# Performance work log

Measured on AMD Instinct MI355X. Metric: run time of the kernel, lower is better.

The kernel has to match this reference:

```python
import jax, jax.numpy as jnp
import numpy as np

N_NODES = 25000
N_HEDGES = 12500
NNZ = 400000
C_IN = 128
HID = 256
HEADS = 4
DH = HID // HEADS  # 64
NQ = 1             # number_queries
LN_EPS = 1e-5


def _layer_norm(x, g, b):
    m = jnp.mean(x, axis=-1, keepdims=True)
    v = jnp.mean((x - m) ** 2, axis=-1, keepdims=True)
    return (x - m) * jax.lax.rsqrt(v + LN_EPS) * g + b


def _block(x_src, src, tgt, n_tgt, K, Qw, V, ln0_g, ln0_b, ln1_g, ln1_b, W1, W2):
    """AllSetTransformerBlock: segment-softmax multi-head attention + LN/MLP.

    x_src: [N_src, C]; K,V: [H, C, DH]; Qw: [H, NQ, DH]; src,tgt: [E] int.
    torch.sparse.softmax over dim=1 == softmax over each target's incident
    sources (unspecified entries are -inf), so a segment softmax is exact.
    """
    xK = jnp.einsum('nc,hcd->hnd', x_src, K)        # [H, N, DH]
    alpha = jnp.einsum('hqd,hnd->nhq', Qw, xK)      # [N, H, NQ]
    a = alpha[src]                                   # [E, H, NQ] gather per incidence
    m = jax.ops.segment_max(a, tgt, num_segments=n_tgt)
    e = jnp.exp(a - m[tgt])
    den = jax.ops.segment_sum(e, tgt, num_segments=n_tgt)
    attn = e / den[tgt]                              # [E, H, NQ]
    v = jnp.einsum('nc,hcd->nhd', x_src, V)[src]     # [E, H, DH]
    w = attn[:, :, :, None] * v[:, :, None, :]       # [E, H, NQ, DH]
    out = jax.ops.segment_sum(w, tgt, num_segments=n_tgt)  # [T, H, NQ, DH]
    out = out + Qw[None]                             # residual with queries
    out = out.transpose(0, 2, 1, 3).reshape(n_tgt, NQ, HID)
    x = _layer_norm(out, ln0_g, ln0_b)
    h = jnp.maximum(x @ W1, 0.0) @ W2                # MLP: Linear-ReLU-Linear, no bias
    x = _layer_norm(x + jnp.maximum(h, 0.0), ln1_g, ln1_b)
    return x.sum(axis=1)                             # [T, HID]


def setup_inputs() -> dict:
    key = jax.random.key(0)
    ks = jax.random.split(key, 12)
    # injective linear-congruential index generation -> unique (node, hedge) pairs,
    # matching a coalesced sparse incidence matrix
    P = 15485863
    lin = (np.arange(NNZ, dtype=np.int64) * P) % (N_NODES * N_HEDGES)
    node_idx = jnp.asarray(lin // N_HEDGES, dtype=jnp.int64)
    hedge_idx = jnp.asarray(lin % N_HEDGES, dtype=jnp.int64)
    s = 0.05
    w = lambda k, shape: jax.random.normal(k, shape, jnp.float32) * s
    d = {
        'x0': jax.random.normal(ks[0], (N_NODES, C_IN), jnp.float32),
        'node_idx': node_idx,
        'hedge_idx': hedge_idx,
        'n_hedges': N_HEDGES,
        'v2e_K': w(ks[1], (HEADS, C_IN, DH)),
        'v2e_Q': w(ks[2], (HEADS, NQ, DH)),
        'v2e_V': w(ks[3], (HEADS, C_IN, DH)),
        'v2e_W1': w(ks[4], (HID, HID)),
        'v2e_W2': w(ks[5], (HID, HID)),
        'v2e_ln0_g': jnp.ones(HID, jnp.float32), 'v2e_ln0_b': jnp.zeros(HID, jnp.float32),
        'v2e_ln1_g': jnp.ones(HID, jnp.float32), 'v2e_ln1_b': jnp.zeros(HID, jnp.float32),
        'e2v_K': w(ks[6], (HEADS, HID, DH)),
        'e2v_Q': w(ks[7], (HEADS, NQ, DH)),
        'e2v_V': w(ks[8], (HEADS, HID, DH)),
        'e2v_W1': w(ks[9], (HID, HID)),
        'e2v_W2': w(ks[10], (HID, HID)),
        'e2v_ln0_g': jnp.ones(HID, jnp.float32), 'e2v_ln0_b': jnp.zeros(HID, jnp.float32),
        'e2v_ln1_g': jnp.ones(HID, jnp.float32), 'e2v_ln1_b': jnp.zeros(HID, jnp.float32),
    }
    return d


def reference(x0, node_idx, hedge_idx, n_hedges,
              v2e_K, v2e_Q, v2e_V, v2e_W1, v2e_W2,
              v2e_ln0_g, v2e_ln0_b, v2e_ln1_g, v2e_ln1_b,
              e2v_K, e2v_Q, e2v_V, e2v_W1, e2v_W2,
              e2v_ln0_g, e2v_ln0_b, e2v_ln1_g, e2v_ln1_b):
    n_nodes = x0.shape[0]
    # vertex -> hyperedge (neighborhood = B^T: targets are hyperedges)
    x1 = jax.nn.relu(_block(x0, node_idx, hedge_idx, n_hedges,
                            v2e_K, v2e_Q, v2e_V,
                            v2e_ln0_g, v2e_ln0_b, v2e_ln1_g, v2e_ln1_b,
                            v2e_W1, v2e_W2))
    # hyperedge -> vertex (neighborhood = B: targets are nodes)
    x0_out = jax.nn.relu(_block(x1, hedge_idx, node_idx, n_nodes,
                                e2v_K, e2v_Q, e2v_V,
                                e2v_ln0_g, e2v_ln0_b, e2v_ln1_g, e2v_ln1_b,
                                e2v_W1, e2v_W2))
    return x0_out, x1
```

## Files before the change

### kernel.cpp

```cpp
#include <hip/hip_runtime.h>
#include <hip/hip_bf16.h>

#define N_NODES_C 25000
#define N_HEDGES_C 12500
#define NNZ_C 400000
#define C_IN_C 128
#define HID_C 256
#define LN_EPS_C 1e-5f
#define CSR_STRIDE 64

typedef unsigned short ushort_t;
typedef __attribute__((ext_vector_type(8))) short short8;
typedef __attribute__((ext_vector_type(4))) float f32x4;

union U4S8 { uint4 u; short8 s; };

__device__ __forceinline__ float ldsel(const void* p, size_t i, bool f32) {
    return f32 ? ((const float*)p)[i] : __bfloat162float(((const __hip_bfloat16*)p)[i]);
}
__device__ __forceinline__ int ldidx(const void* p, size_t i, bool i64) {
    return i64 ? (int)((const long long*)p)[i] : ((const int*)p)[i];
}
__device__ __forceinline__ ushort_t bfbits(float f) {
    union { float f; unsigned u; } v; v.f = f;
    unsigned r = v.u + 0x7FFF + ((v.u >> 16) & 1);
    return (ushort_t)(r >> 16);
}
__device__ __forceinline__ float blo(unsigned u) {
    union { unsigned u; float f; } v; v.u = u << 16; return v.f;
}
__device__ __forceinline__ float bhi(unsigned u) {
    union { unsigned u; float f; } v; v.u = u & 0xFFFF0000u; return v.f;
}

#define INIT_GRID 148
__global__ void __launch_bounds__(256)
init_kernel(const unsigned* __restrict__ x0w, const unsigned* __restrict__ idxw,
            int* __restrict__ flags, unsigned* __restrict__ cnts,
            unsigned* __restrict__ vb32, unsigned* __restrict__ ea32) {
    int bid = blockIdx.x;
    if (bid == 0) {
        __shared__ int cnt[2];
        int t = threadIdx.x;
        if (t < 2) cnt[t] = 0;
        __syncthreads();
        int c0 = 0, c1 = 0;
        for (int k = 0; k < 4; k++) {
            unsigned w = x0w[t * 4 + k];
            unsigned elo = (w >> 7) & 0xFF;
            if (elo >= 100 && elo <= 134) c0++;
            if (idxw[2 * (t * 4 + k) + 1] == 0) c1++;
        }
        atomicAdd(&cnt[0], c0);
        atomicAdd(&cnt[1], c1);
        __syncthreads();
        if (t == 0) {
            flags[0] = (cnt[0] < 512) ? 1 : 0;
            flags[1] = (cnt[1] >= 512) ? 1 : 0;
        }
        return;
    }
    int i = (bid - 1) * 256 + threadIdx.x;
    if (i < 37500) { cnts[i] = 0u; return; }
    i -= 37500;
    if (i < 128) { vb32[25000 * 128 + i] = 0u; return; }
    i -= 128;
    if (i < 4) ea32[100000 + i] = 0u;
}

#define FILL_CHUNK 1024
#define FILL_NCHUNK ((NNZ_C + FILL_CHUNK - 1) / FILL_CHUNK)
#define FILL_BLOCKS (8 * FILL_NCHUNK)
#define HSLICE_SZ 1563
#define NSLICE_SZ 3125
#define PREP_TOTAL 364544
#define PREP_BLOCKS ((PREP_TOTAL + 255) / 256)
#define PF_GRID (FILL_BLOCKS + PREP_BLOCKS)

__global__ void __launch_bounds__(256)
prep_fill_kernel(const void* __restrict__ node_idx, const void* __restrict__ hedge_idx,
                 int* __restrict__ fill_h, int* __restrict__ fill_n,
                 ushort_t* __restrict__ scsr_h, ushort_t* __restrict__ scsr_n,
                 const void* __restrict__ K1, const void* __restrict__ Q1,
                 const void* __restrict__ V1,
                 const void* __restrict__ K2, const void* __restrict__ Q2,
                 const void* __restrict__ V2,
                 const void* __restrict__ W1a, const void* __restrict__ W2a,
                 const void* __restrict__ W1b, const void* __restrict__ W2b,
                 const void* __restrict__ G0a, const void* __restrict__ B0a,
                 const void* __restrict__ G1a, const void* __restrict__ B1a,
                 const void* __restrict__ G0b, const void* __restrict__ B0b,
                 const void* __restrict__ G1b, const void* __restrict__ B1b,
                 const int* __restrict__ flags,
                 float* __restrict__ kq1, float* __restrict__ kq2,
                 ushort_t* __restrict__ Vt1b, ushort_t* __restrict__ Vt2b,
                 ushort_t* __restrict__ W1tA, ushort_t* __restrict__ W2tA,
                 ushort_t* __restrict__ W1tB, ushort_t* __restrict__ W2tB,
                 float* __restrict__ qgb1, float* __restrict__ ep1,
                 float* __restrict__ qgb2, float* __restrict__ ep2) {
    if (blockIdx.x < FILL_BLOCKS) {
        bool i64 = flags[1] != 0;
        int s = blockIdx.x & 7;
        int chunk = blockIdx.x >> 3;
        int e0 = chunk * FILL_CHUNK;
        int e1 = e0 + FILL_CHUNK; if (e1 > NNZ_C) e1 = NNZ_C;
        int hlo = s * HSLICE_SZ, hhi = hlo + HSLICE_SZ;
        int nlo = s * NSLICE_SZ, nhi = nlo + NSLICE_SZ;
        for (int e = e0 + threadIdx.x; e < e1; e += 256) {
            int nd = ldidx(node_idx, e, i64);
            int he = ldidx(hedge_idx, e, i64);
            if (he >= hlo && he < hhi) {
                int p = atomicAdd(&fill_h[he], 1);
                if (p < CSR_STRIDE) scsr_h[(he << 6) + p] = (ushort_t)nd;
            }
            if (nd >= nlo && nd < nhi) {
                int p = atomicAdd(&fill_n[nd], 1);
                if (p < CSR_STRIDE) scsr_n[(nd << 6) + p] = (ushort_t)he;
            }
        }
        return;
    }
    bool f32 = flags[0] != 0;
    size_t i = (size_t)(blockIdx.x - FILL_BLOCKS) * 256 + threadIdx.x;
    if (i >= PREP_TOTAL) return;
    if (i < 512) {
        int h = (int)(i >> 7), c = (int)(i & 127);
        float s = 0.f;
        for (int d = 0; d < 64; d++)
            s += ldsel(K1, (size_t)(h * 128 + c) * 64 + d, f32) * ldsel(Q1, h * 64 + d, f32);
        kq1[h * 128 + c] = s;
        return;
    }
    i -= 512;
    if (i < 1024) {
        int h = (int)(i >> 8), c = (int)(i & 255);
        float s = 0.f;
        for (int d = 0; d < 64; d++)
            s += ldsel(K2, (size_t)(h * 256 + c) * 64 + d, f32) * ldsel(Q2, h * 64 + d, f32);
        kq2[h * 256 + c] = s;
        return;
    }
    i -= 1024;
    if (i < 32768) {
        int j = (int)(i >> 7), c = (int)(i & 127);
        int h = j >> 6, d = j & 63;
        Vt1b[i] = bfbits(ldsel(V1, (size_t)(h * 128 + c) * 64 + d, f32));
        return;
    }
    i -= 32768;
    if (i < 65536) {
        int j = (int)(i >> 8), c = (int)(i & 255);
        int h = j >> 6, d = j & 63;
        Vt2b[i] = bfbits(ldsel(V2, (size_t)(h * 256 + c) * 64 + d, f32));
        return;
    }
    i -= 65536;
    if (i < 65536) { int n = (int)(i >> 8), k = (int)(i & 255);
        W1tA[i] = bfbits(ldsel(W1a, (size_t)k * 256 + n, f32)); return; }
    i -= 65536;
    if (i < 65536) { int n = (int)(i >> 8), k = (int)(i & 255);
        W2tA[i] = bfbits(ldsel(W2a, (size_t)k * 256 + n, f32)); return; }
    i -= 65536;
    if (i < 65536) { int n = (int)(i >> 8), k = (int)(i & 255);
        W1tB[i] = bfbits(ldsel(W1b, (size_t)k * 256 + n, f32)); return; }
    i -= 65536;
    if (i < 65536) { int n = (int)(i >> 8), k = (int)(i & 255);
        W2tB[i] = bfbits(ldsel(W2b, (size_t)k * 256 + n, f32)); return; }
    i -= 65536;
    {
        int which = (int)(i >> 8);
        int j = (int)(i & 255);
        const void* src; float* dst;
        switch (which) {
            case 0: src = Q1;  dst = qgb1;       break;
            case 1: src = G0a; dst = qgb1 + 256; break;
            case 2: src = B0a; dst = qgb1 + 512; break;
            case 3: src = G1a; dst = ep1;        break;
            case 4: src = B1a; dst = ep1 + 256;  break;
            case 5: src = Q2;  dst = qgb2;       break;
            case 6: src = G0b; dst = qgb2 + 256; break;
            case 7: src = B0b; dst = qgb2 + 512; break;
            case 8: src = G1b; dst = ep2;        break;
            default: src = B1b; dst = ep2 + 256;  break;
        }
        dst[j] = ldsel(src, j, f32);
    }
}

__global__ void __launch_bounds__(256)
gemm_x0_kernel(const void* __restrict__ x0, const int* __restrict__ flags,
               const ushort_t* __restrict__ Bt, ushort_t* __restrict__ C,
               int M, int K, const float* __restrict__ kq, float* __restrict__ ea) {
    __shared__ ushort_t As[64 * 72];
    __shared__ ushort_t Bs[128 * 72];
    __shared__ float kqs[512];
    bool f32 = flags[0] != 0;
    int tid = threadIdx.x;
    int w = tid >> 6, lane = tid & 63;
    int l15 = lane & 15, kg = lane >> 4;
    int wr = w >> 1, wc = w & 1;
    int row0 = blockIdx.x * 64, col0 = blockIdx.y * 128;
    bool doEa = (blockIdx.y == 0);
    kqs[tid] = kq[tid];
    kqs[256 + tid] = kq[256 + tid];
    __syncthreads();
    f32x4 acc[2][4] = {{{0.f,0.f,0.f,0.f},{0.f,0.f,0.f,0.f},{0.f,0.f,0.f,0.f},{0.f,0.f,0.f,0.f}},
                       {{0.f,0.f,0.f,0.f},{0.f,0.f,0.f,0.f},{0.f,0.f,0.f,0.f},{0.f,0.f,0.f,0.f}}};
    float hd[2][4] = {{0.f,0.f,0.f,0.f},{0.f,0.f,0.f,0.f}};
    int r_ = tid >> 3, ch = tid & 7;
    for (int k0 = 0; k0 < K; k0 += 64) {
#pragma unroll
        for (int p = 0; p < 2; p++) {
            int r = p * 32 + r_;
            uint4 av = {0u,0u,0u,0u};
            int gr = row0 + r;
            if (gr < M) {
                float fv[8];
                if (!f32) {
                    av = *(const uint4*)((const ushort_t*)x0 + (size_t)gr * K + k0 + ch * 8);
                    if (doEa) {
                        unsigned* uw = (unsigned*)&av;
#pragma unroll
                        for (int jj = 0; jj < 4; jj++) { fv[2 * jj] = blo(uw[jj]); fv[2 * jj + 1] = bhi(uw[jj]); }
                    }
                } else {
                    const float* ap = (const float*)x0 + (size_t)gr * K + k0 + ch * 8;
                    float4 f0 = *(const float4*)ap;
                    float4 f1 = *(const float4*)(ap + 4);
                    av.x = (unsigned)bfbits(f0.x) | ((unsigned)bfbits(f0.y) << 16);
                    av.y = (unsigned)bfbits(f0.z) | ((unsigned)bfbits(f0.w) << 16);
                    av.z = (unsigned)bfbits(f1.x) | ((unsigned)bfbits(f1.y) << 16);
                    av.w = (unsigned)bfbits(f1.z) | ((unsigned)bfbits(f1.w) << 16);
                    if (doEa) {
                        fv[0] = f0.x; fv[1] = f0.y; fv[2] = f0.z; fv[3] = f0.w;
                        fv[4] = f1.x; fv[5] = f1.y; fv[6] = f1.z; fv[7] = f1.w;
                    }
                }
                if (doEa) {
                    int c = k0 + ch * 8;
#pragma unroll
                    for (int h = 0; h < 4; h++) {
                        float s = 0.f;
#pragma unroll
                        for (int j = 0; j < 8; j++) s += fv[j] * kqs[h * 128 + c + j];
                        hd[p][h] += s;
                    }
                }
            }
            *(uint4*)&As[r * 72 + ch * 8] = av;
        }
#pragma unroll
        for (int p = 0; p < 4; p++) {
            int i = p * 256 + tid;
            int r2 = i >> 3, c2 = i & 7;
            uint4 bv = *(const uint4*)(Bt + (size_t)(col0 + r2) * K + k0 + c2 * 8);
            *(uint4*)&Bs[r2 * 72 + c2 * 8] = bv;
        }
        __syncthreads();
#pragma unroll
        for (int kk = 0; kk < 2; kk++) {
            U4S8 a0_, a1_;
            a0_.u = *(const uint4*)&As[(32 * wr + l15) * 72 + kk * 32 + kg * 8];
            a1_.u = *(const uint4*)&As[(32 * wr + 16 + l15) * 72 + kk * 32 + kg * 8];
#pragma unroll
            for (int n = 0; n < 4; n++) {
                U4S8 b; b.u = *(const uint4*)&Bs[(64 * wc + 16 * n + l15) * 72 + kk * 32 + kg * 8];
                acc[0][n] = __builtin_amdgcn_mfma_f32_16x16x32_bf16(a0_.s, b.s, acc[0][n], 0, 0, 0);
                acc[1][n] = __builtin_amdgcn_mfma_f32_16x16x32_bf16(a1_.s, b.s, acc[1][n], 0, 0, 0);
            }
        }
        __syncthreads();
    }
#pragma unroll
    for (int m = 0; m < 2; m++) {
#pragma unroll
        for (int n = 0; n < 4; n++) {
#pragma unroll
            for (int rr = 0; rr < 4; rr++) {
                int row = row0 + 32 * wr + 16 * m + kg * 4 + rr;
                if (row < M)
                    C[(size_t)row * 256 + col0 + 64 * wc + 16 * n + l15] = bfbits(acc[m][n][rr]);
            }
        }
    }
    if (doEa) {
#pragma unroll
        for (int p = 0; p < 2; p++) {
#pragma unroll
            for (int msk = 1; msk < 8; msk <<= 1) {
                hd[p][0] += __shfl_xor(hd[p][0], msk);
                hd[p][1] += __shfl_xor(hd[p][1], msk);
                hd[p][2] += __shfl_xor(hd[p][2], msk);
                hd[p][3] += __shfl_xor(hd[p][3], msk);
            }
            if (ch == 0) {
                int row = row0 + p * 32 + r_;
                if (row < M) {
                    float4 o;
                    o.x = __expf(hd[p][0]); o.y = __expf(hd[p][1]);
                    o.z = __expf(hd[p][2]); o.w = __expf(hd[p][3]);
                    *(float4*)(ea + (size_t)row * 4) = o;
                }
            }
        }
    }
}

#define LOADB4(SRC, KO) { \
    bv0 = *(const uint4*)((SRC) + (size_t)rb * 256 + (KO) + cb * 8); \
    bv1 = *(const uint4*)((SRC) + (size_t)(rb + 64) * 256 + (KO) + cb * 8); \
    bv2 = *(const uint4*)((SRC) + (size_t)(rb + 128) * 256 + (KO) + cb * 8); \
    bv3 = *(const uint4*)((SRC) + (size_t)(rb + 192) * 256 + (KO) + cb * 8); }
#define WRITEB4() { \
    *(uint4*)&Bs[rb * 72 + cb * 8] = bv0; \
    *(uint4*)&Bs[(rb + 64) * 72 + cb * 8] = bv1; \
    *(uint4*)&Bs[(rb + 128) * 72 + cb * 8] = bv2; \
    *(uint4*)&Bs[(rb + 192) * 72 + cb * 8] = bv3; }

__global__ void __launch_bounds__(512)
fused_mlp_ln_kernel(const ushort_t* __restrict__ A, const ushort_t* __restrict__ W1t,
                    const ushort_t* __restrict__ W2t, const float* __restrict__ ep,
                    float* __restrict__ outF, int M,
                    const ushort_t* __restrict__ Vt2b, const float* __restrict__ kq,
                    ushort_t* __restrict__ vbOut, float* __restrict__ eaOut,
                    unsigned* __restrict__ zrow, float* __restrict__ zea) {
    __shared__ ushort_t Bs[256 * 72];
    __shared__ ushort_t hs[32 * 264];
    __shared__ float s1s[32][4];
    __shared__ float s2s[32][4];
    __shared__ float kqs[1024];
    ushort_t* As = hs;
    int tid = threadIdx.x;
    int w = tid >> 6, lane = tid & 63;
    int l15 = lane & 15, kg = lane >> 4;
    int wr = w >> 2, wc = w & 3;
    int row0 = blockIdx.x * 32;
    bool dir1 = (Vt2b != nullptr);
    if (dir1) { kqs[tid] = kq[tid]; kqs[512 + tid] = kq[512 + tid]; }
    f32x4 acc[4] = {{0.f,0.f,0.f,0.f},{0.f,0.f,0.f,0.f},{0.f,0.f,0.f,0.f},{0.f,0.f,0.f,0.f}};
    int rb = tid >> 3, cb = tid & 7;
    bool doA = tid < 256;
    int gr = row0 + rb;
    uint4 av = {0u,0u,0u,0u};
    uint4 bv0, bv1, bv2, bv3;
    LOADB4(W1t, 0);
    if (doA && gr < M) av = *(const uint4*)(A + (size_t)gr * 256 + cb * 8);
    for (int k0 = 0; k0 < 256; k0 += 64) {
        WRITEB4();
        if (doA) *(uint4*)&As[rb * 72 + cb * 8] = av;
        __syncthreads();
        if (k0 < 192) {
            LOADB4(W1t, k0 + 64);
            if (doA && gr < M) av = *(const uint4*)(A + (size_t)gr * 256 + (k0 + 64) + cb * 8);
        }
#pragma unroll
        for (int kk = 0; kk < 2; kk++) {
            U4S8 a0_;
            a0_.u = *(const uint4*)&As[(16 * wr + l15) * 72 + kk * 32 + kg * 8];
#pragma unroll
            for (int n = 0; n < 4; n++) {
                U4S8 b; b.u = *(const uint4*)&Bs[(64 * wc + 16 * n + l15) * 72 + kk * 32 + kg * 8];
                acc[n] = __builtin_amdgcn_mfma_f32_16x16x32_bf16(a0_.s, b.s, acc[n], 0, 0, 0);
            }
        }
        __syncthreads();
    }
    LOADB4(W2t, 0);
#pragma unroll
    for (int n = 0; n < 4; n++) {
#pragma unroll
        for (int rr = 0; rr < 4; rr++) {
            int br = 16 * wr + kg * 4 + rr;
            hs[br * 264 + 64 * wc + 16 * n + l15] = bfbits(fmaxf(acc[n][rr], 0.f));
            acc[n][rr] = 0.f;
        }
    }
    __syncthreads();
    for (int k0 = 0; k0 < 256; k0 += 64) {
        WRITEB4();
        __syncthreads();
        if (k0 < 192) LOADB4(W2t, k0 + 64);
#pragma unroll
        for (int kk = 0; kk < 2; kk++) {
            U4S8 a0_;
            a0_.u = *(const uint4*)&hs[(16 * wr + l15) * 264 + k0 + kk * 32 + kg * 8];
#pragma unroll
            for (int n = 0; n < 4; n++) {
                U4S8 b; b.u = *(const uint4*)&Bs[(64 * wc + 16 * n + l15) * 72 + kk * 32 + kg * 8];
                acc[n] = __builtin_amdgcn_mfma_f32_16x16x32_bf16(a0_.s, b.s, acc[n], 0, 0, 0);
            }
        }
        __syncthreads();
    }
    float ym[4][4];
#pragma unroll
    for (int rr = 0; rr < 4; rr++) {
        int br = 16 * wr + kg * 4 + rr;
        int grow = row0 + br;
        float ls1 = 0.f;
#pragma unroll
        for (int n = 0; n < 4; n++) {
            int col = 64 * wc + 16 * n + l15;
            float xv = 0.f;
            if (grow < M) xv = blo((unsigned)A[(size_t)grow * 256 + col]);
            float yv = xv + fmaxf(acc[n][rr], 0.f);
            ym[n][rr] = yv;
            ls1 += yv;
        }
#pragma unroll
        for (int msk = 1; msk < 16; msk <<= 1) ls1 += __shfl_xor(ls1, msk);
        if (l15 == 0) s1s[br][wc] = ls1;
    }
    __syncthreads();
    float mean_[4];
#pragma unroll
    for (int rr = 0; rr < 4; rr++) {
        int br = 16 * wr + kg * 4 + rr;
        float mn = (s1s[br][0] + s1s[br][1] + s1s[br][2] + s1s[br][3]) * (1.f / 256.f);
        mean_[rr] = mn;
        float ls2 = 0.f;
#pragma unroll
        for (int n = 0; n < 4; n++) {
            float d = ym[n][rr] - mn;
            ls2 += d * d;
        }
#pragma unroll
        for (int msk = 1; msk < 16; msk <<= 1) ls2 += __shfl_xor(ls2, msk);
        if (l15 == 0) s2s[br][wc] = ls2;
    }
    __syncthreads();
#pragma unroll
    for (int rr = 0; rr < 4; rr++) {
        int br = 16 * wr + kg * 4 + rr;
        int grow = row0 + br;
        float var = (s2s[br][0] + s2s[br][1] + s2s[br][2] + s2s[br][3]) * (1.f / 256.f);
        float rs = rsqrtf(var + LN_EPS_C);
#pragma unroll
        for (int n = 0; n < 4; n++) {
            int col = 64 * wc + 16 * n + l15;
            float rv = (ym[n][rr] - mean_[rr]) * rs * ep[col] + ep[256 + col];
            rv = fmaxf(rv, 0.f);
            if (grow < M) outF[(size_t)grow * 256 + col] = rv;
            if (dir1) hs[br * 264 + col] = bfbits(rv);
        }
    }
    if (!dir1) return;
#pragma unroll
    for (int n = 0; n < 4; n++)
#pragma unroll
        for (int rr = 0; rr < 4; rr++) acc[n][rr] = 0.f;
    LOADB4(Vt2b, 0);
    __syncthreads();
    if (blockIdx.x == 0) {
        if (tid < 128) zrow[tid] = 0u;
        else if (tid < 132) zea[tid - 128] = 0.f;
    }
    {
        int rrow = tid >> 4, rch = tid & 15;
        float h0 = 0.f, h1 = 0.f, h2 = 0.f, h3 = 0.f;
#pragma unroll
        for (int q = 0; q < 2; q++) {
            uint4 xv = *(const uint4*)&hs[rrow * 264 + rch * 16 + q * 8];
            const unsigned* uw = (const unsigned*)&xv;
#pragma unroll
            for (int jj = 0; jj < 4; jj++) {
                float xl = blo(uw[jj]), xh = bhi(uw[jj]);
                int c = rch * 16 + q * 8 + jj * 2;
                h0 += xl * kqs[c]       + xh * kqs[c + 1];
                h1 += xl * kqs[256 + c] + xh * kqs[256 + c + 1];
                h2 += xl * kqs[512 + c] + xh * kqs[512 + c + 1];
                h3 += xl * kqs[768 + c] + xh * kqs[768 + c + 1];
            }
        }
#pragma unroll
        for (int msk = 1; msk < 16; msk <<= 1) {
            h0 += __shfl_xor(h0, msk); h1 += __shfl_xor(h1, msk);
            h2 += __shfl_xor(h2, msk); h3 += __shfl_xor(h3, msk);
        }
        int grow = row0 + rrow;
        if (rch == 0 && grow < M) {
            float4 o;
            o.x = __expf(h0); o.y = __expf(h1); o.z = __expf(h2); o.w = __expf(h3);
            *(float4*)(eaOut + (size_t)grow * 4) = o;
        }
    }
    for (int k0 = 0; k0 < 256; k0 += 64) {
        WRITEB4();
        __syncthreads();
        if (k0 < 192) LOADB4(Vt2b, k0 + 64);
#pragma unroll
        for (int kk = 0; kk < 2; kk++) {
            U4S8 a0_;
            a0_.u = *(const uint4*)&hs[(16 * wr + l15) * 264 + k0 + kk * 32 + kg * 8];
#pragma unroll
            for (int n = 0; n < 4; n++) {
                U4S8 b; b.u = *(const uint4*)&Bs[(64 * wc + 16 * n + l15) * 72 + kk * 32 + kg * 8];
                acc[n] = __builtin_amdgcn_mfma_f32_16x16x32_bf16(a0_.s, b.s, acc[n], 0, 0, 0);
            }
        }
        __syncthreads();
    }
#pragma unroll
    for (int n = 0; n < 4; n++) {
#pragma unroll
        for (int rr = 0; rr < 4; rr++) {
            int row = row0 + 16 * wr + kg * 4 + rr;
            if (row < M)
                vbOut[(size_t)row * 256 + 64 * wc + 16 * n + l15] = bfbits(acc[n][rr]);
        }
    }
}

#define DECL_BANKD(B) float e##B##0, e##B##1, e##B##2, e##B##3; \
                      uint2 u##B##0, u##B##1, u##B##2, u##B##3;
#define ISSUED1(B, n, sl) { \
    int _i = ((sl) < cnt) ? __shfl(myidx, (sl)) : dummyIdx; \
    int _o = _i << 9; \
    u##B##n = *(const uint2*)(vbL + _o); \
    e##B##n = *(const float*)(eaL + (_o >> 5)); }
#define ISSUED4(B, base) ISSUED1(B,0,(base)) ISSUED1(B,1,(base)+1) ISSUED1(B,2,(base)+2) ISSUED1(B,3,(base)+3)
#define EATD1(B, n) { \
    float wgt = e##B##n; \
    den += wgt; \
    a0 += wgt * blo(u##B##n.x); a1 += wgt * bhi(u##B##n.x); \
    a2 += wgt * blo(u##B##n.y); a3 += wgt * bhi(u##B##n.y); }
#define EATD4(B) EATD1(B,0) EATD1(B,1) EATD1(B,2) EATD1(B,3)

__global__ void __launch_bounds__(256)
attn_ln_kernel(const int* __restrict__ cnts, const ushort_t* __restrict__ scsr,
               const char* __restrict__ eaB, const char* __restrict__ vbB,
               const float* __restrict__ qgb, uint2* __restrict__ xlnbf2,
               int dummyIdx) {
    int wid = (blockIdx.x << 2) + (threadIdx.x >> 6);
    int lane = threadIdx.x & 63;
    const char* vbL = vbB + (lane << 3);
    const char* eaL = eaB + ((lane >> 4) << 2);
    int cnt = cnts[wid];
    if (cnt > CSR_STRIDE) cnt = CSR_STRIDE;
    int myidx = (int)scsr[(wid << 6) + lane];
    float a0 = 0.f, a1 = 0.f, a2 = 0.f, a3 = 0.f, den = 0.f;
    int kr = (cnt + 3) & ~3;
    DECL_BANKD(A)
    DECL_BANKD(B)
    if (kr > 0) { ISSUED4(A, 0) }
    for (int k = 0; k < kr; k += 8) {
        int kb = k + 4;
        bool hasB = kb < kr;
        if (hasB) { ISSUED4(B, kb) }
        EATD4(A)
        int ka = k + 8;
        if (ka < kr) { ISSUED4(A, ka) }
        if (hasB) { EATD4(B) }
    }
    float inv = (den > 0.f) ? (1.f / den) : 0.f;
    int c0i = lane << 2;
    float o0 = a0 * inv + qgb[c0i];
    float o1 = a1 * inv + qgb[c0i + 1];
    float o2 = a2 * inv + qgb[c0i + 2];
    float o3 = a3 * inv + qgb[c0i + 3];
    float part = o0 + o1 + o2 + o3;
#pragma unroll
    for (int m = 32; m; m >>= 1) part += __shfl_xor(part, m);
    float mean = part * (1.f / 256.f);
    float d0 = o0 - mean, d1 = o1 - mean, d2 = o2 - mean, d3 = o3 - mean;
    float p2 = d0 * d0 + d1 * d1 + d2 * d2 + d3 * d3;
#pragma unroll
    for (int m = 32; m; m >>= 1) p2 += __shfl_xor(p2, m);
    float rs = rsqrtf(p2 * (1.f / 256.f) + LN_EPS_C);
    float r0 = d0 * rs * qgb[256 + c0i] + qgb[512 + c0i];
    float r1 = d1 * rs * qgb[256 + c0i + 1] + qgb[512 + c0i + 1];
    float r2 = d2 * rs * qgb[256 + c0i + 2] + qgb[512 + c0i + 2];
    float r3 = d3 * rs * qgb[256 + c0i + 3] + qgb[512 + c0i + 3];
    uint2 outw;
    outw.x = ((unsigned)bfbits(r1) << 16) | bfbits(r0);
    outw.y = ((unsigned)bfbits(r3) << 16) | bfbits(r2);
    xlnbf2[(size_t)wid * 64 + lane] = outw;
}

#define OFF_KQ1   0
#define OFF_KQ2   2048
#define OFF_QGB1  6144
#define OFF_EP1   9216
#define OFF_QGB2  11264
#define OFF_EP2   14336
#define OFF_EA    16384
#define OFF_VT1B  416512
#define OFF_VT2B  482048
#define OFF_W1TA  613120
#define OFF_W2TA  744192
#define OFF_W1TB  875264
#define OFF_W2TB  1006336
#define OFF_VB    1137408
#define OFF_XLNBF 13937920
#define OFF_FLAGS 45937920
#define OFF_FILLH 45937952
#define OFF_FILLN 45987952
#define OFF_SCSRH 46087952
#define OFF_SCSRN 47687952

extern "C" void kernel_launch(void* const* d_in, const int* in_sizes, int n_in,
                              void* d_out, int out_size, void* d_ws, size_t ws_size,
                              hipStream_t stream) {
    const void* x0        = d_in[0];
    const void* node_idx  = d_in[1];
    const void* hedge_idx = d_in[2];
    const void* v2e_K  = d_in[4];
    const void* v2e_Q  = d_in[5];
    const void* v2e_V  = d_in[6];
    const void* v2e_W1 = d_in[7];
    const void* v2e_W2 = d_in[8];
    const void* v2e_ln0_g = d_in[9];
    const void* v2e_ln0_b = d_in[10];
    const void* v2e_ln1_g = d_in[11];
    const void* v2e_ln1_b = d_in[12];
    const void* e2v_K  = d_in[13];
    const void* e2v_Q  = d_in[14];
    const void* e2v_V  = d_in[15];
    const void* e2v_W1 = d_in[16];
    const void* e2v_W2 = d_in[17];
    const void* e2v_ln0_g = d_in[18];
    const void* e2v_ln0_b = d_in[19];
    const void* e2v_ln1_g = d_in[20];
    const void* e2v_ln1_b = d_in[21];

    float* out = (float*)d_out;
    float* out_x0 = out;
    float* out_x1 = out + (size_t)N_NODES_C * HID_C;

    char* base = (char*)d_ws;
    float*    kq1   = (float*)(base + OFF_KQ1);
    float*    kq2   = (float*)(base + OFF_KQ2);
    float*    qgb1  = (float*)(base + OFF_QGB1);
    float*    ep1   = (float*)(base + OFF_EP1);
    float*    qgb2  = (float*)(base + OFF_QGB2);
    float*    ep2   = (float*)(base + OFF_EP2);
    float*    ea    = (float*)(base + OFF_EA);
    ushort_t* Vt1b  = (ushort_t*)(base + OFF_VT1B);
    ushort_t* Vt2b  = (ushort_t*)(base + OFF_VT2B);
    ushort_t* W1tA  = (ushort_t*)(base + OFF_W1TA);
    ushort_t* W2tA  = (ushort_t*)(base + OFF_W2TA);
    ushort_t* W1tB  = (ushort_t*)(base + OFF_W1TB);
    ushort_t* W2tB  = (ushort_t*)(base + OFF_W2TB);
    ushort_t* vb    = (ushort_t*)(base + OFF_VB);
    ushort_t* xlnbf = (ushort_t*)(base + OFF_XLNBF);
    int*      flags = (int*)(base + OFF_FLAGS);
    int*      fill_h = (int*)(base + OFF_FILLH);
    int*      fill_n = (int*)(base + OFF_FILLN);
    ushort_t* scsr_h = (ushort_t*)(base + OFF_SCSRH);
    ushort_t* scsr_n = (ushort_t*)(base + OFF_SCSRN);

    init_kernel<<<INIT_GRID, 256, 0, stream>>>(
        (const unsigned*)x0, (const unsigned*)node_idx, flags,
        (unsigned*)fill_h, (unsigned*)vb, (unsigned*)ea);

    prep_fill_kernel<<<PF_GRID, 256, 0, stream>>>(
        node_idx, hedge_idx, fill_h, fill_n, scsr_h, scsr_n,
        v2e_K, v2e_Q, v2e_V, e2v_K, e2v_Q, e2v_V,
        v2e_W1, v2e_W2, e2v_W1, e2v_W2,
        v2e_ln0_g, v2e_ln0_b, v2e_ln1_g, v2e_ln1_b,
        e2v_ln0_g, e2v_ln0_b, e2v_ln1_g, e2v_ln1_b,
        flags, kq1, kq2, Vt1b, Vt2b, W1tA, W2tA, W1tB, W2tB,
        qgb1, ep1, qgb2, ep2);

    gemm_x0_kernel<<<dim3((N_NODES_C + 63) / 64, 2), 256, 0, stream>>>(
        x0, flags, Vt1b, vb, N_NODES_C, C_IN_C, kq1, ea);
    attn_ln_kernel<<<N_HEDGES_C / 4, 256, 0, stream>>>(
        fill_h, scsr_h, (const char*)ea, (const char*)vb, qgb1, (uint2*)xlnbf,
        25000);
    fused_mlp_ln_kernel<<<(N_HEDGES_C + 31) / 32, 512, 0, stream>>>(
        xlnbf, W1tA, W2tA, ep1, out_x1, N_HEDGES_C,
        Vt2b, kq2, vb, ea,
        (unsigned*)vb + 12500 * 128, ea + 50000);

    attn_ln_kernel<<<N_NODES_C / 4, 256, 0, stream>>>(
        fill_n, scsr_n, (const char*)ea, (const char*)vb, qgb2, (uint2*)xlnbf,
        12500);
    fused_mlp_ln_kernel<<<(N_NODES_C + 31) / 32, 512, 0, stream>>>(
        xlnbf, W1tB, W2tB, ep2, out_x0, N_NODES_C,
        nullptr, nullptr, nullptr, nullptr, nullptr, nullptr);
}
```

Baseline: 182.8 us.

## Fuse segment-attention+LayerNorm into the MLP kernel, keeping normalized rows in LDS

Merges the attention/LN kernel and the MLP/LN kernel into one, so each 512-thread block first computes attention for its 32 targets (4 per wave) and writes the normalized bf16 rows into shared memory, then runs the two GEMMs and the second LN from there. This removes the global round trip of the xlnbf intermediate and two kernel launches. Because the fused kernel now writes next-direction V/ea while other blocks still read them, it uses separate ea2/vb2 buffers to avoid the read-write race. The cost is more LDS per block (extra 32x264 tile), which lowers occupancy, and gather latency is no longer hidden by many small blocks.

```diff
diff --git a/kernel.cpp b/kernel.cpp
--- a/kernel.cpp
+++ b/kernel.cpp
@@ -317,200 +317,6 @@
     *(uint4*)&Bs[(rb + 128) * 72 + cb * 8] = bv2; \
     *(uint4*)&Bs[(rb + 192) * 72 + cb * 8] = bv3; }
 
-__global__ void __launch_bounds__(512)
-fused_mlp_ln_kernel(const ushort_t* __restrict__ A, const ushort_t* __restrict__ W1t,
-                    const ushort_t* __restrict__ W2t, const float* __restrict__ ep,
-                    float* __restrict__ outF, int M,
-                    const ushort_t* __restrict__ Vt2b, const float* __restrict__ kq,
-                    ushort_t* __restrict__ vbOut, float* __restrict__ eaOut,
-                    unsigned* __restrict__ zrow, float* __restrict__ zea) {
-    __shared__ ushort_t Bs[256 * 72];
-    __shared__ ushort_t hs[32 * 264];
-    __shared__ float s1s[32][4];
-    __shared__ float s2s[32][4];
-    __shared__ float kqs[1024];
-    ushort_t* As = hs;
-    int tid = threadIdx.x;
-    int w = tid >> 6, lane = tid & 63;
-    int l15 = lane & 15, kg = lane >> 4;
-    int wr = w >> 2, wc = w & 3;
-    int row0 = blockIdx.x * 32;
-    bool dir1 = (Vt2b != nullptr);
-    if (dir1) { kqs[tid] = kq[tid]; kqs[512 + tid] = kq[512 + tid]; }
-    f32x4 acc[4] = {{0.f,0.f,0.f,0.f},{0.f,0.f,0.f,0.f},{0.f,0.f,0.f,0.f},{0.f,0.f,0.f,0.f}};
-    int rb = tid >> 3, cb = tid & 7;
-    bool doA = tid < 256;
-    int gr = row0 + rb;
-    uint4 av = {0u,0u,0u,0u};
-    uint4 bv0, bv1, bv2, bv3;
-    LOADB4(W1t, 0);
-    if (doA && gr < M) av = *(const uint4*)(A + (size_t)gr * 256 + cb * 8);
-    for (int k0 = 0; k0 < 256; k0 += 64) {
-        WRITEB4();
-        if (doA) *(uint4*)&As[rb * 72 + cb * 8] = av;
-        __syncthreads();
-        if (k0 < 192) {
-            LOADB4(W1t, k0 + 64);
-            if (doA && gr < M) av = *(const uint4*)(A + (size_t)gr * 256 + (k0 + 64) + cb * 8);
-        }
-#pragma unroll
-        for (int kk = 0; kk < 2; kk++) {
-            U4S8 a0_;
-            a0_.u = *(const uint4*)&As[(16 * wr + l15) * 72 + kk * 32 + kg * 8];
-#pragma unroll
-            for (int n = 0; n < 4; n++) {
-                U4S8 b; b.u = *(const uint4*)&Bs[(64 * wc + 16 * n + l15) * 72 + kk * 32 + kg * 8];
-                acc[n] = __builtin_amdgcn_mfma_f32_16x16x32_bf16(a0_.s, b.s, acc[n], 0, 0, 0);
-            }
-        }
-        __syncthreads();
-    }
-    LOADB4(W2t, 0);
-#pragma unroll
-    for (int n = 0; n < 4; n++) {
-#pragma unroll
-        for (int rr = 0; rr < 4; rr++) {
-            int br = 16 * wr + kg * 4 + rr;
-            hs[br * 264 + 64 * wc + 16 * n + l15] = bfbits(fmaxf(acc[n][rr], 0.f));
-            acc[n][rr] = 0.f;
-        }
-    }
-    __syncthreads();
-    for (int k0 = 0; k0 < 256; k0 += 64) {
-        WRITEB4();
-        __syncthreads();
-        if (k0 < 192) LOADB4(W2t, k0 + 64);
-#pragma unroll
-        for (int kk = 0; kk < 2; kk++) {
-            U4S8 a0_;
-            a0_.u = *(const uint4*)&hs[(16 * wr + l15) * 264 + k0 + kk * 32 + kg * 8];
-#pragma unroll
-            for (int n = 0; n < 4; n++) {
-                U4S8 b; b.u = *(const uint4*)&Bs[(64 * wc + 16 * n + l15) * 72 + kk * 32 + kg * 8];
-                acc[n] = __builtin_amdgcn_mfma_f32_16x16x32_bf16(a0_.s, b.s, acc[n], 0, 0, 0);
-            }
-        }
-        __syncthreads();
-    }
-    float ym[4][4];
-#pragma unroll
-    for (int rr = 0; rr < 4; rr++) {
-        int br = 16 * wr + kg * 4 + rr;
-        int grow = row0 + br;
-        float ls1 = 0.f;
-#pragma unroll
-        for (int n = 0; n < 4; n++) {
-            int col = 64 * wc + 16 * n + l15;
-            float xv = 0.f;
-            if (grow < M) xv = blo((unsigned)A[(size_t)grow * 256 + col]);
-            float yv = xv + fmaxf(acc[n][rr], 0.f);
-            ym[n][rr] = yv;
-            ls1 += yv;
-        }
-#pragma unroll
-        for (int msk = 1; msk < 16; msk <<= 1) ls1 += __shfl_xor(ls1, msk);
-        if (l15 == 0) s1s[br][wc] = ls1;
-    }
-    __syncthreads();
-    float mean_[4];
-#pragma unroll
-    for (int rr = 0; rr < 4; rr++) {
-        int br = 16 * wr + kg * 4 + rr;
-        float mn = (s1s[br][0] + s1s[br][1] + s1s[br][2] + s1s[br][3]) * (1.f / 256.f);
-        mean_[rr] = mn;
-        float ls2 = 0.f;
-#pragma unroll
-        for (int n = 0; n < 4; n++) {
-            float d = ym[n][rr] - mn;
-            ls2 += d * d;
-        }
-#pragma unroll
-        for (int msk = 1; msk < 16; msk <<= 1) ls2 += __shfl_xor(ls2, msk);
-        if (l15 == 0) s2s[br][wc] = ls2;
-    }
-    __syncthreads();
-#pragma unroll
-    for (int rr = 0; rr < 4; rr++) {
-        int br = 16 * wr + kg * 4 + rr;
-        int grow = row0 + br;
-        float var = (s2s[br][0] + s2s[br][1] + s2s[br][2] + s2s[br][3]) * (1.f / 256.f);
-        float rs = rsqrtf(var + LN_EPS_C);
-#pragma unroll
-        for (int n = 0; n < 4; n++) {
-            int col = 64 * wc + 16 * n + l15;
-            float rv = (ym[n][rr] - mean_[rr]) * rs * ep[col] + ep[256 + col];
-            rv = fmaxf(rv, 0.f);
-            if (grow < M) outF[(size_t)grow * 256 + col] = rv;
-            if (dir1) hs[br * 264 + col] = bfbits(rv);
-        }
-    }
-    if (!dir1) return;
-#pragma unroll
-    for (int n = 0; n < 4; n++)
-#pragma unroll
-        for (int rr = 0; rr < 4; rr++) acc[n][rr] = 0.f;
-    LOADB4(Vt2b, 0);
-    __syncthreads();
-    if (blockIdx.x == 0) {
-        if (tid < 128) zrow[tid] = 0u;
-        else if (tid < 132) zea[tid - 128] = 0.f;
-    }
-    {
-        int rrow = tid >> 4, rch = tid & 15;
-        float h0 = 0.f, h1 = 0.f, h2 = 0.f, h3 = 0.f;
-#pragma unroll
-        for (int q = 0; q < 2; q++) {
-            uint4 xv = *(const uint4*)&hs[rrow * 264 + rch * 16 + q * 8];
-            const unsigned* uw = (const unsigned*)&xv;
-#pragma unroll
-            for (int jj = 0; jj < 4; jj++) {
-                float xl = blo(uw[jj]), xh = bhi(uw[jj]);
-                int c = rch * 16 + q * 8 + jj * 2;
-                h0 += xl * kqs[c]       + xh * kqs[c + 1];
-                h1 += xl * kqs[256 + c] + xh * kqs[256 + c + 1];
-                h2 += xl * kqs[512 + c] + xh * kqs[512 + c + 1];
-                h3 += xl * kqs[768 + c] + xh * kqs[768 + c + 1];
-            }
-        }
-#pragma unroll
-        for (int msk = 1; msk < 16; msk <<= 1) {
-            h0 += __shfl_xor(h0, msk); h1 += __shfl_xor(h1, msk);
-            h2 += __shfl_xor(h2, msk); h3 += __shfl_xor(h3, msk);
-        }
-        int grow = row0 + rrow;
-        if (rch == 0 && grow < M) {
-            float4 o;
-            o.x = __expf(h0); o.y = __expf(h1); o.z = __expf(h2); o.w = __expf(h3);
-            *(float4*)(eaOut + (size_t)grow * 4) = o;
-        }
-    }
-    for (int k0 = 0; k0 < 256; k0 += 64) {
-        WRITEB4();
-        __syncthreads();
-        if (k0 < 192) LOADB4(Vt2b, k0 + 64);
-#pragma unroll
-        for (int kk = 0; kk < 2; kk++) {
-            U4S8 a0_;
-            a0_.u = *(const uint4*)&hs[(16 * wr + l15) * 264 + k0 + kk * 32 + kg * 8];
-#pragma unroll
-            for (int n = 0; n < 4; n++) {
-                U4S8 b; b.u = *(const uint4*)&Bs[(64 * wc + 16 * n + l15) * 72 + kk * 32 + kg * 8];
-                acc[n] = __builtin_amdgcn_mfma_f32_16x16x32_bf16(a0_.s, b.s, acc[n], 0, 0, 0);
-            }
-        }
-        __syncthreads();
-    }
-#pragma unroll
-    for (int n = 0; n < 4; n++) {
-#pragma unroll
-        for (int rr = 0; rr < 4; rr++) {
-            int row = row0 + 16 * wr + kg * 4 + rr;
-            if (row < M)
-                vbOut[(size_t)row * 256 + 64 * wc + 16 * n + l15] = bfbits(acc[n][rr]);
-        }
-    }
-}
-
 #define DECL_BANKD(B) float e##B##0, e##B##1, e##B##2, e##B##3; \
                       uint2 u##B##0, u##B##1, u##B##2, u##B##3;
 #define ISSUED1(B, n, sl) { \
@@ -526,55 +332,242 @@
     a2 += wgt * blo(u##B##n.y); a3 += wgt * bhi(u##B##n.y); }
 #define EATD4(B) EATD1(B,0) EATD1(B,1) EATD1(B,2) EATD1(B,3)
 
-__global__ void __launch_bounds__(256)
-attn_ln_kernel(const int* __restrict__ cnts, const ushort_t* __restrict__ scsr,
-               const char* __restrict__ eaB, const char* __restrict__ vbB,
-               const float* __restrict__ qgb, uint2* __restrict__ xlnbf2,
-               int dummyIdx) {
-    int wid = (blockIdx.x << 2) + (threadIdx.x >> 6);
-    int lane = threadIdx.x & 63;
-    const char* vbL = vbB + (lane << 3);
-    const char* eaL = eaB + ((lane >> 4) << 2);
-    int cnt = cnts[wid];
-    if (cnt > CSR_STRIDE) cnt = CSR_STRIDE;
-    int myidx = (int)scsr[(wid << 6) + lane];
-    float a0 = 0.f, a1 = 0.f, a2 = 0.f, a3 = 0.f, den = 0.f;
-    int kr = (cnt + 3) & ~3;
-    DECL_BANKD(A)
-    DECL_BANKD(B)
-    if (kr > 0) { ISSUED4(A, 0) }
-    for (int k = 0; k < kr; k += 8) {
-        int kb = k + 4;
-        bool hasB = kb < kr;
-        if (hasB) { ISSUED4(B, kb) }
-        EATD4(A)
-        int ka = k + 8;
-        if (ka < kr) { ISSUED4(A, ka) }
-        if (hasB) { EATD4(B) }
-    }
-    float inv = (den > 0.f) ? (1.f / den) : 0.f;
-    int c0i = lane << 2;
-    float o0 = a0 * inv + qgb[c0i];
-    float o1 = a1 * inv + qgb[c0i + 1];
-    float o2 = a2 * inv + qgb[c0i + 2];
-    float o3 = a3 * inv + qgb[c0i + 3];
-    float part = o0 + o1 + o2 + o3;
-#pragma unroll
-    for (int m = 32; m; m >>= 1) part += __shfl_xor(part, m);
-    float mean = part * (1.f / 256.f);
-    float d0 = o0 - mean, d1 = o1 - mean, d2 = o2 - mean, d3 = o3 - mean;
-    float p2 = d0 * d0 + d1 * d1 + d2 * d2 + d3 * d3;
-#pragma unroll
-    for (int m = 32; m; m >>= 1) p2 += __shfl_xor(p2, m);
-    float rs = rsqrtf(p2 * (1.f / 256.f) + LN_EPS_C);
-    float r0 = d0 * rs * qgb[256 + c0i] + qgb[512 + c0i];
-    float r1 = d1 * rs * qgb[256 + c0i + 1] + qgb[512 + c0i + 1];
-    float r2 = d2 * rs * qgb[256 + c0i + 2] + qgb[512 + c0i + 2];
-    float r3 = d3 * rs * qgb[256 + c0i + 3] + qgb[512 + c0i + 3];
-    uint2 outw;
-    outw.x = ((unsigned)bfbits(r1) << 16) | bfbits(r0);
-    outw.y = ((unsigned)bfbits(r3) << 16) | bfbits(r2);
-    xlnbf2[(size_t)wid * 64 + lane] = outw;
+__global__ void __launch_bounds__(512)
+fused_attn_mlp_kernel(const int* __restrict__ cnts, const ushort_t* __restrict__ scsr,
+                      const char* __restrict__ eaB, const char* __restrict__ vbB,
+                      const float* __restrict__ qgb, int dummyIdx,
+                      const ushort_t* __restrict__ W1t, const ushort_t* __restrict__ W2t,
+                      const float* __restrict__ ep,
+                      float* __restrict__ outF, int M,
+                      const ushort_t* __restrict__ Vt2b, const float* __restrict__ kq,
+                      ushort_t* __restrict__ vbOut, float* __restrict__ eaOut,
+                      unsigned* __restrict__ zrow, float* __restrict__ zea) {
+    __shared__ ushort_t Bs[256 * 72];
+    __shared__ ushort_t hs[32 * 264];
+    __shared__ ushort_t xs[32 * 264];
+    __shared__ float s1s[32][4];
+    __shared__ float s2s[32][4];
+    __shared__ float kqs[1024];
+    int tid = threadIdx.x;
+    int w = tid >> 6, lane = tid & 63;
+    int l15 = lane & 15, kg = lane >> 4;
+    int wr = w >> 2, wc = w & 3;
+    int row0 = blockIdx.x * 32;
+    bool dir1 = (Vt2b != nullptr);
+    if (dir1) { kqs[tid] = kq[tid]; kqs[512 + tid] = kq[512 + tid]; }
+    int rb = tid >> 3, cb = tid & 7;
+    uint4 bv0, bv1, bv2, bv3;
+    LOADB4(W1t, 0);
+    {
+        const char* vbL = vbB + (lane << 3);
+        const char* eaL = eaB + ((lane >> 4) << 2);
+        for (int t = 0; t < 4; t++) {
+            int tl = (w << 2) + t;
+            int wid = row0 + tl;
+            int cnt = 0, myidx = dummyIdx;
+            if (wid < M) {
+                cnt = cnts[wid];
+                if (cnt > CSR_STRIDE) cnt = CSR_STRIDE;
+                myidx = (int)scsr[(wid << 6) + lane];
+            }
+            float a0 = 0.f, a1 = 0.f, a2 = 0.f, a3 = 0.f, den = 0.f;
+            int kr = (cnt + 3) & ~3;
+            DECL_BANKD(A)
+            DECL_BANKD(B)
+            if (kr > 0) { ISSUED4(A, 0) }
+            for (int k = 0; k < kr; k += 8) {
+                int kb = k + 4;
+                bool hasB = kb < kr;
+                if (hasB) { ISSUED4(B, kb) }
+                EATD4(A)
+                int ka = k + 8;
+                if (ka < kr) { ISSUED4(A, ka) }
+                if (hasB) { EATD4(B) }
+            }
+            float inv = (den > 0.f) ? (1.f / den) : 0.f;
+            int c0i = lane << 2;
+            float o0 = a0 * inv + qgb[c0i];
+            float o1 = a1 * inv + qgb[c0i + 1];
+            float o2 = a2 * inv + qgb[c0i + 2];
+            float o3 = a3 * inv + qgb[c0i + 3];
+            float part = o0 + o1 + o2 + o3;
+#pragma unroll
+            for (int m = 32; m; m >>= 1) part += __shfl_xor(part, m);
+            float mean = part * (1.f / 256.f);
+            float d0 = o0 - mean, d1 = o1 - mean, d2 = o2 - mean, d3 = o3 - mean;
+            float p2 = d0 * d0 + d1 * d1 + d2 * d2 + d3 * d3;
+#pragma unroll
+            for (int m = 32; m; m >>= 1) p2 += __shfl_xor(p2, m);
+            float rs = rsqrtf(p2 * (1.f / 256.f) + LN_EPS_C);
+            float r0 = d0 * rs * qgb[256 + c0i] + qgb[512 + c0i];
+            float r1 = d1 * rs * qgb[256 + c0i + 1] + qgb[512 + c0i + 1];
+            float r2 = d2 * rs * qgb[256 + c0i + 2] + qgb[512 + c0i + 2];
+            float r3 = d3 * rs * qgb[256 + c0i + 3] + qgb[512 + c0i + 3];
+            uint2 outw;
+            outw.x = ((unsigned)bfbits(r1) << 16) | bfbits(r0);
+            outw.y = ((unsigned)bfbits(r3) << 16) | bfbits(r2);
+            *(uint2*)&xs[tl * 264 + c0i] = outw;
+        }
+    }
+    f32x4 acc[4] = {{0.f,0.f,0.f,0.f},{0.f,0.f,0.f,0.f},{0.f,0.f,0.f,0.f},{0.f,0.f,0.f,0.f}};
+    for (int k0 = 0; k0 < 256; k0 += 64) {
+        WRITEB4();
+        __syncthreads();
+        if (k0 < 192) LOADB4(W1t, k0 + 64);
+#pragma unroll
+        for (int kk = 0; kk < 2; kk++) {
+            U4S8 a0_;
+            a0_.u = *(const uint4*)&xs[(16 * wr + l15) * 264 + k0 + kk * 32 + kg * 8];
+#pragma unroll
+            for (int n = 0; n < 4; n++) {
+                U4S8 b; b.u = *(const uint4*)&Bs[(64 * wc + 16 * n + l15) * 72 + kk * 32 + kg * 8];
+                acc[n] = __builtin_amdgcn_mfma_f32_16x16x32_bf16(a0_.s, b.s, acc[n], 0, 0, 0);
+            }
+        }
+        __syncthreads();
+    }
+    LOADB4(W2t, 0);
+#pragma unroll
+    for (int n = 0; n < 4; n++) {
+#pragma unroll
+        for (int rr = 0; rr < 4; rr++) {
+            int br = 16 * wr + kg * 4 + rr;
+            hs[br * 264 + 64 * wc + 16 * n + l15] = bfbits(fmaxf(acc[n][rr], 0.f));
+            acc[n][rr] = 0.f;
+        }
+    }
+    __syncthreads();
+    for (int k0 = 0; k0 < 256; k0 += 64) {
+        WRITEB4();
+        __syncthreads();
+        if (k0 < 192) LOADB4(W2t, k0 + 64);
+#pragma unroll
+        for (int kk = 0; kk < 2; kk++) {
+            U4S8 a0_;
+            a0_.u = *(const uint4*)&hs[(16 * wr + l15) * 264 + k0 + kk * 32 + kg * 8];
+#pragma unroll
+            for (int n = 0; n < 4; n++) {
+                U4S8 b; b.u = *(const uint4*)&Bs[(64 * wc + 16 * n + l15) * 72 + kk * 32 + kg * 8];
+                acc[n] = __builtin_amdgcn_mfma_f32_16x16x32_bf16(a0_.s, b.s, acc[n], 0, 0, 0);
+            }
+        }
+        __syncthreads();
+    }
+    float ym[4][4];
+#pragma unroll
+    for (int rr = 0; rr < 4; rr++) {
+        int br = 16 * wr + kg * 4 + rr;
+        float ls1 = 0.f;
+#pragma unroll
+        for (int n = 0; n < 4; n++) {
+            int col = 64 * wc + 16 * n + l15;
+            float xv = blo((unsigned)xs[br * 264 + col]);
+            float yv = xv + fmaxf(acc[n][rr], 0.f);
+            ym[n][rr] = yv;
+            ls1 += yv;
+        }
+#pragma unroll
+        for (int msk = 1; msk < 16; msk <<= 1) ls1 += __shfl_xor(ls1, msk);
+        if (l15 == 0) s1s[br][wc] = ls1;
+    }
+    __syncthreads();
+    float mean_[4];
+#pragma unroll
+    for (int rr = 0; rr < 4; rr++) {
+        int br = 16 * wr + kg * 4 + rr;
+        float mn = (s1s[br][0] + s1s[br][1] + s1s[br][2] + s1s[br][3]) * (1.f / 256.f);
+        mean_[rr] = mn;
+        float ls2 = 0.f;
+#pragma unroll
+        for (int n = 0; n < 4; n++) {
+            float d = ym[n][rr] - mn;
+            ls2 += d * d;
+        }
+#pragma unroll
+        for (int msk = 1; msk < 16; msk <<= 1) ls2 += __shfl_xor(ls2, msk);
+        if (l15 == 0) s2s[br][wc] = ls2;
+    }
+    __syncthreads();
+#pragma unroll
+    for (int rr = 0; rr < 4; rr++) {
+        int br = 16 * wr + kg * 4 + rr;
+        int grow = row0 + br;
+        float var = (s2s[br][0] + s2s[br][1] + s2s[br][2] + s2s[br][3]) * (1.f / 256.f);
+        float rs = rsqrtf(var + LN_EPS_C);
+#pragma unroll
+        for (int n = 0; n < 4; n++) {
+            int col = 64 * wc + 16 * n + l15;
+            float rv = (ym[n][rr] - mean_[rr]) * rs * ep[col] + ep[256 + col];
+            rv = fmaxf(rv, 0.f);
+            if (grow < M) outF[(size_t)grow * 256 + col] = rv;
+            if (dir1) hs[br * 264 + col] = bfbits(rv);
+        }
+    }
+    if (!dir1) return;
+#pragma unroll
+    for (int n = 0; n < 4; n++)
+#pragma unroll
+        for (int rr = 0; rr < 4; rr++) acc[n][rr] = 0.f;
+    LOADB4(Vt2b, 0);
+    __syncthreads();
+    if (blockIdx.x == 0) {
+        if (tid < 128) zrow[tid] = 0u;
+        else if (tid < 132) zea[tid - 128] = 0.f;
+    }
+    {
+        int rrow = tid >> 4, rch = tid & 15;
+        float h0 = 0.f, h1 = 0.f, h2 = 0.f, h3 = 0.f;
+#pragma unroll
+        for (int q = 0; q < 2; q++) {
+            uint4 xv = *(const uint4*)&hs[rrow * 264 + rch * 16 + q * 8];
+            const unsigned* uw = (const unsigned*)&xv;
+#pragma unroll
+            for (int jj = 0; jj < 4; jj++) {
+                float xl = blo(uw[jj]), xh = bhi(uw[jj]);
+                int c = rch * 16 + q * 8 + jj * 2;
+                h0 += xl * kqs[c]       + xh * kqs[c + 1];
+                h1 += xl * kqs[256 + c] + xh * kqs[256 + c + 1];
+                h2 += xl * kqs[512 + c] + xh * kqs[512 + c + 1];
+                h3 += xl * kqs[768 + c] + xh * kqs[768 + c + 1];
+            }
+        }
+#pragma unroll
+        for (int msk = 1; msk < 16; msk <<= 1) {
+            h0 += __shfl_xor(h0, msk); h1 += __shfl_xor(h1, msk);
+            h2 += __shfl_xor(h2, msk); h3 += __shfl_xor(h3, msk);
+        }
+        int grow = row0 + rrow;
+        if (rch == 0 && grow < M) {
+            float4 o;
+            o.x = __expf(h0); o.y = __expf(h1); o.z = __expf(h2); o.w = __expf(h3);
+            *(float4*)(eaOut + (size_t)grow * 4) = o;
+        }
+    }
+    for (int k0 = 0; k0 < 256; k0 += 64) {
+        WRITEB4();
+        __syncthreads();
+        if (k0 < 192) LOADB4(Vt2b, k0 + 64);
+#pragma unroll
+        for (int kk = 0; kk < 2; kk++) {
+            U4S8 a0_;
+            a0_.u = *(const uint4*)&hs[(16 * wr + l15) * 264 + k0 + kk * 32 + kg * 8];
+#pragma unroll
+            for (int n = 0; n < 4; n++) {
+                U4S8 b; b.u = *(const uint4*)&Bs[(64 * wc + 16 * n + l15) * 72 + kk * 32 + kg * 8];
+                acc[n] = __builtin_amdgcn_mfma_f32_16x16x32_bf16(a0_.s, b.s, acc[n], 0, 0, 0);
+            }
+        }
+        __syncthreads();
+    }
+#pragma unroll
+    for (int n = 0; n < 4; n++) {
+#pragma unroll
+        for (int rr = 0; rr < 4; rr++) {
+            int row = row0 + 16 * wr + kg * 4 + rr;
+            if (row < M)
+                vbOut[(size_t)row * 256 + 64 * wc + 16 * n + l15] = bfbits(acc[n][rr]);
+        }
+    }
 }
 
 #define OFF_KQ1   0
@@ -591,7 +584,8 @@
 #define OFF_W1TB  875264
 #define OFF_W2TB  1006336
 #define OFF_VB    1137408
-#define OFF_XLNBF 13937920
+#define OFF_EA2   13937920
+#define OFF_VB2   14145536
 #define OFF_FLAGS 45937920
 #define OFF_FILLH 45937952
 #define OFF_FILLN 45987952
@@ -635,6 +629,7 @@
     float*    qgb2  = (float*)(base + OFF_QGB2);
     float*    ep2   = (float*)(base + OFF_EP2);
     float*    ea    = (float*)(base + OFF_EA);
+    float*    ea2   = (float*)(base + OFF_EA2);
     ushort_t* Vt1b  = (ushort_t*)(base + OFF_VT1B);
     ushort_t* Vt2b  = (ushort_t*)(base + OFF_VT2B);
     ushort_t* W1tA  = (ushort_t*)(base + OFF_W1TA);
@@ -642,7 +637,7 @@
     ushort_t* W1tB  = (ushort_t*)(base + OFF_W1TB);
     ushort_t* W2tB  = (ushort_t*)(base + OFF_W2TB);
     ushort_t* vb    = (ushort_t*)(base + OFF_VB);
-    ushort_t* xlnbf = (ushort_t*)(base + OFF_XLNBF);
+    ushort_t* vb2   = (ushort_t*)(base + OFF_VB2);
     int*      flags = (int*)(base + OFF_FLAGS);
     int*      fill_h = (int*)(base + OFF_FILLH);
     int*      fill_n = (int*)(base + OFF_FILLN);
@@ -664,18 +659,15 @@
 
     gemm_x0_kernel<<<dim3((N_NODES_C + 63) / 64, 2), 256, 0, stream>>>(
         x0, flags, Vt1b, vb, N_NODES_C, C_IN_C, kq1, ea);
-    attn_ln_kernel<<<N_HEDGES_C / 4, 256, 0, stream>>>(
-        fill_h, scsr_h, (const char*)ea, (const char*)vb, qgb1, (uint2*)xlnbf,
-        25000);
-    fused_mlp_ln_kernel<<<(N_HEDGES_C + 31) / 32, 512, 0, stream>>>(
-        xlnbf, W1tA, W2tA, ep1, out_x1, N_HEDGES_C,
-        Vt2b, kq2, vb, ea,
-        (unsigned*)vb + 12500 * 128, ea + 50000);
-
-    attn_ln_kernel<<<N_NODES_C / 4, 256, 0, stream>>>(
-        fill_n, scsr_n, (const char*)ea, (const char*)vb, qgb2, (uint2*)xlnbf,
-        12500);
-    fused_mlp_ln_kernel<<<(N_NODES_C + 31) / 32, 512, 0, stream>>>(
-        xlnbf, W1tB, W2tB, ep2, out_x0, N_NODES_C,
+
+    fused_attn_mlp_kernel<<<(N_HEDGES_C + 31) / 32, 512, 0, stream>>>(
+        fill_h, scsr_h, (const char*)ea, (const char*)vb, qgb1, 25000,
+        W1tA, W2tA, ep1, out_x1, N_HEDGES_C,
+        Vt2b, kq2, vb2, ea2,
+        (unsigned*)vb2 + 12500 * 128, ea2 + 50000);
+
+    fused_attn_mlp_kernel<<<(N_NODES_C + 31) / 32, 512, 0, stream>>>(
+        fill_n, scsr_n, (const char*)ea2, (const char*)vb2, qgb2, 12500,
+        W1tB, W2tB, ep2, out_x0, N_NODES_C,
         nullptr, nullptr, nullptr, nullptr, nullptr, nullptr);
 }
```

Measured after the change: 181.2 us. No clear change (-0.9%).
